# Performance work log

Hardware: AMD Instinct MI355X
Metric: run time of the kernel (lower is better)

The kernel has to match this reference:

```python
import jax, jax.numpy as jnp
import numpy as np

NUM_COMPONENTS = 8
STRIDE, PADDING, OUTPUT_PADDING, K = 2, 1, 0, 4


def get_comp_mat(n):
    # Cayley-Dickson construction: entry [i, j] = +/- component index of the
    # weight multiplying input component j to produce output component i.
    A = np.array([[0]])
    while A.shape[0] < n:
        m = A.shape[0]
        A = np.vstack([np.hstack([A, -(A + m)]), np.hstack([A + m, A])])
    return A


def setup_inputs() -> dict:
    key = jax.random.key(0)
    k1, k2, k3 = jax.random.split(key, 3)
    B, Cin, Cout, H = 8, 512, 256, 64
    c_in, c_out = Cin // NUM_COMPONENTS, Cout // NUM_COMPONENTS
    x = jax.random.normal(k1, (B, Cin, H, H), jnp.float32)
    # per-component ConvTranspose2d weights, torch layout [C_in, C_out, kH, kW]
    W = jax.random.normal(k2, (NUM_COMPONENTS, c_in, c_out, K, K), jnp.float32) * 0.05
    b = jax.random.normal(k3, (NUM_COMPONENTS, c_out), jnp.float32) * 0.05
    return {"x": x, "W": W, "b": b}


def reference(x, W, b):
    n = NUM_COMPONENTS
    comp = get_comp_mat(n)                 # static [n, n] signed component table
    signs = jnp.asarray(np.where(comp < 0, -1.0, 1.0), x.dtype)
    idx = np.abs(comp)                     # which sub-conv weight to use
    c_in, c_out, kh, kw = W.shape[1:]
    # Fuse the n^2 transpose convs into ONE block transpose conv:
    # Kbig[j*c_in:(j+1)*c_in, i*c_out:(i+1)*c_out] = sign[i,j] * W[idx[i,j]]
    Wsel = W[idx] * signs[:, :, None, None, None, None]          # [ni, nj, c_in, c_out, kh, kw]
    Wbig = jnp.transpose(Wsel, (1, 2, 0, 3, 4, 5)).reshape(n * c_in, n * c_out, kh, kw)
    bbig = jnp.einsum('ij,ijc->ic', signs, b[idx]).reshape(n * c_out)
    # torch ConvTranspose2d == conv with input dilated by stride and flipped kernel
    rhs = jnp.flip(Wbig, (2, 3)).transpose(1, 0, 2, 3)           # OIHW
    pad = K - 1 - PADDING
    out = jax.lax.conv_general_dilated(
        x, rhs, window_strides=(1, 1),
        padding=((pad, pad + OUTPUT_PADDING), (pad, pad + OUTPUT_PADDING)),
        lhs_dilation=(STRIDE, STRIDE),
        dimension_numbers=('NCHW', 'OIHW', 'NCHW'))
    return out + bbig[None, :, None, None]
```

## Files before the change

kernel.cpp:

```cpp
#include <hip/hip_runtime.h>
#include <hip/hip_bf16.h>

typedef unsigned short ushort_t;
typedef __attribute__((ext_vector_type(8))) short short8;
typedef __attribute__((ext_vector_type(4))) float f32x4;

#define NCOMP    8
#define CIN      512
#define COUT     256
#define H        64
#define HP       66
#define OHW      128
#define NB       8

__device__ const int d_idx8[8][8] = {
    {0,1,2,1,4,3,2,3},
    {1,0,3,2,5,4,1,2},
    {2,1,0,1,6,5,4,3},
    {3,2,1,0,7,6,5,4},
    {4,3,2,3,0,1,2,1},
    {5,4,1,2,1,0,3,2},
    {6,5,4,3,2,1,0,1},
    {7,6,5,4,3,2,1,0}};

__device__ const int kh_tab[2][2] = {{1,3},{0,2}};
__device__ const int dh_tab[2][2] = {{0,-1},{1,0}};

__global__ void prep_x(const float* __restrict__ x, ushort_t* __restrict__ xpadT) {
    __shared__ ushort_t tile[32][33];
    const int ih  = blockIdx.x;
    const int iw0 = (blockIdx.y & 1) * 32;
    const int ic0 = (blockIdx.y >> 1) * 32;
    const int b   = blockIdx.z;
    const int t   = threadIdx.x;

    for (int e = t; e < 1024; e += 256) {
        int icl = e >> 5, iwl = e & 31;
        float v = x[(((size_t)b * CIN + ic0 + icl) * H + ih) * H + iw0 + iwl];
        __hip_bfloat16 h = __float2bfloat16(v);
        tile[icl][iwl] = *(ushort_t*)&h;
    }
    __syncthreads();
    const int iwl = t >> 3, g = t & 7;
    ushort4 v;
    v.x = tile[g * 4 + 0][iwl];
    v.y = tile[g * 4 + 1][iwl];
    v.z = tile[g * 4 + 2][iwl];
    v.w = tile[g * 4 + 3][iwl];
    ushort_t* dst = xpadT + (((size_t)b * HP + ih + 1) * HP + iw0 + iwl + 1) * CIN + ic0 + g * 4;
    *(ushort4*)dst = v;
}

__global__ void prep_w(const float* __restrict__ W, const float* __restrict__ bias,
                       ushort_t* __restrict__ Abf, float* __restrict__ bbig) {
    const int t = blockIdx.x * blockDim.x + threadIdx.x;
    if (t < 4 * 64 * 256 * 32) {
        int kin = t & 31;
        int oc  = (t >> 5) & 255;
        int ks  = (t >> 13) & 63;
        int cls = t >> 19;
        int k  = ks * 32 + kin;
        int a  = k >> 10, c = (k >> 9) & 1, ic = k & 511;
        int ph = cls >> 1, pw = cls & 1;
        int kh = kh_tab[ph][a], kw = kh_tab[pw][c];
        int i = oc >> 5, co = oc & 31;
        int j = ic >> 6, ci = ic & 63;
        float s = (i >= j) ? 1.0f : -1.0f;
        float v = s * W[(((size_t)(d_idx8[i][j] * 64 + ci) * 32 + co) * 4 + kh) * 4 + kw];
        __hip_bfloat16 h = __float2bfloat16(v);
        Abf[t] = *(ushort_t*)&h;
    }
    if (t < COUT) {
        int i = t >> 5, co = t & 31;
        float acc = 0.0f;
        for (int j = 0; j < NCOMP; ++j)
            acc += ((i >= j) ? 1.0f : -1.0f) * bias[d_idx8[i][j] * 32 + co];
        bbig[t] = acc;
    }
}

__device__ __forceinline__ void async16(void* lds_dst, const void* g_src) {
    __builtin_amdgcn_global_load_lds(
        (const __attribute__((address_space(1))) unsigned int*)g_src,
        (__attribute__((address_space(3))) unsigned int*)lds_dst,
        16, 0, 0);
}

__launch_bounds__(256)
__global__ void htconv_mfma(const ushort_t* __restrict__ xpadT,
                            const ushort_t* __restrict__ Abf,
                            const float* __restrict__ bbig,
                            float* __restrict__ out) {
    __shared__ __align__(16) ushort_t smem[8192];
    char* sb = (char*)smem;

    const int t     = threadIdx.x;
    const int ntile = blockIdx.x;
    const int mtile = blockIdx.y;
    const int cls   = blockIdx.z & 3;
    const int b     = blockIdx.z >> 2;
    const int ph = cls >> 1, pw = cls & 1;
    const int ohh0 = ntile * 2;

    const int srcc = (((t & 3) ^ ((t >> 3) & 3)) * 8);
    const int m_a  = t >> 2;
    const ushort_t* ap = Abf + (((size_t)cls * 64) * 256 + (size_t)mtile * 128 + m_a) * 32 + srcc;

    const int dh0 = dh_tab[ph][0], dh1 = dh_tab[ph][1];
    const int dw0 = dh_tab[pw][0], dw1 = dh_tab[pw][1];
    const int oww = t >> 2;
    const ushort_t* bp[2][2][2];
#pragma unroll
    for (int a = 0; a < 2; ++a) {
        int dh = (a == 0) ? dh0 : dh1;
#pragma unroll
        for (int c = 0; c < 2; ++c) {
            int dw = (c == 0) ? dw0 : dw1;
#pragma unroll
            for (int row = 0; row < 2; ++row) {
                size_t idx = (((size_t)b * HP + ohh0 + row + dh + 1) * HP + oww + dw + 1) * CIN + srcc;
                bp[a][c][row] = xpadT + idx;
            }
        }
    }

    const int lane = t & 63, wave = t >> 6;
    const int wm = wave >> 1, wn = wave & 1;
    const int col = lane & 15, quad = lane >> 4;
    const int soff = (quad ^ ((col >> 1) & 3)) * 16;
    const int aoff = (wm * 64 + col) * 64 + soff;
    const int boff = 8192 + (wn * 64 + col) * 64 + soff;

    f32x4 acc[4][4];
#pragma unroll
    for (int i = 0; i < 4; ++i)
#pragma unroll
        for (int j = 0; j < 4; ++j)
            acc[i][j] = (f32x4){0.f, 0.f, 0.f, 0.f};

#pragma unroll
    for (int a = 0; a < 2; ++a) {
#pragma unroll
        for (int c = 0; c < 2; ++c) {
            const ushort_t* b0 = bp[a][c][0];
            const ushort_t* b1 = bp[a][c][1];
            for (int kk = 0; kk < 16; ++kk) {
                async16(sb + t * 16,         ap);
                async16(sb + 4096 + t * 16,  ap + 2048);
                async16(sb + 8192 + t * 16,  b0);
                async16(sb + 12288 + t * 16, b1);
                ap += 8192; b0 += 32; b1 += 32;
                __syncthreads();

                short8 af[4], bf[4];
#pragma unroll
                for (int s = 0; s < 4; ++s) {
                    af[s] = *(const short8*)(sb + aoff + s * 1024);
                    bf[s] = *(const short8*)(sb + boff + s * 1024);
                }
#pragma unroll
                for (int sm = 0; sm < 4; ++sm)
#pragma unroll
                    for (int sn = 0; sn < 4; ++sn)
                        acc[sm][sn] = __builtin_amdgcn_mfma_f32_16x16x32_bf16(
                            af[sm], bf[sn], acc[sm][sn], 0, 0, 0);
                __syncthreads();
            }
        }
    }

    const int oh = 2 * (ohh0 + wn) + ph;
#pragma unroll
    for (int sm = 0; sm < 4; ++sm) {
#pragma unroll
        for (int r = 0; r < 4; ++r) {
            const int occ = mtile * 128 + wm * 64 + sm * 16 + quad * 4 + r;
            const float bv = bbig[occ];
            float* obase = out + (((size_t)b * COUT + occ) * OHW + oh) * OHW + pw;
#pragma unroll
            for (int sn = 0; sn < 4; ++sn) {
                const int owi = sn * 16 + col;
                obase[2 * owi] = acc[sm][sn][r] + bv;
            }
        }
    }
}

extern "C" void kernel_launch(void* const* d_in, const int* in_sizes, int n_in,
                              void* d_out, int out_size, void* d_ws, size_t ws_size,
                              hipStream_t stream) {
    const float* x    = (const float*)d_in[0];
    const float* W    = (const float*)d_in[1];
    const float* bias = (const float*)d_in[2];
    float* out = (float*)d_out;

    ushort_t* xpadT = (ushort_t*)d_ws;
    ushort_t* Abf   = xpadT + (size_t)NB * HP * HP * CIN;
    float*    bbig  = (float*)(Abf + (size_t)4 * 64 * 256 * 32);

    hipMemsetAsync(xpadT, 0, (size_t)NB * HP * HP * CIN * sizeof(ushort_t), stream);
    prep_x<<<dim3(H, 32, NB), 256, 0, stream>>>(x, xpadT);
    prep_w<<<dim3((4 * 64 * 256 * 32) / 256), 256, 0, stream>>>(W, bias, Abf, bbig);
    htconv_mfma<<<dim3(32, 2, 32), 256, 0, stream>>>(xpadT, Abf, bbig, out);
}
```

Baseline: 372.5 us.

## Double-buffer LDS in conv GEMM main loop and zero only the padding halo

The MFMA main loop now uses two LDS buffers, so the async global-to-LDS loads for the next K-step are issued before the MFMAs on the current step. Each step ends with a single waitcnt and barrier instead of two syncthreads, and B-tile addresses are computed from two base pointers plus an offset. Separately, the full memset of the padded input buffer is replaced by a small kernel that writes zeros only to the halo rows and columns, cutting about 35MB of memset traffic. This doubles LDS use per block, which may lower occupancy.

```diff
diff --git a/kernel.cpp b/kernel.cpp
--- a/kernel.cpp
+++ b/kernel.cpp
@@ -25,6 +25,31 @@
 
 __device__ const int kh_tab[2][2] = {{1,3},{0,2}};
 __device__ const int dh_tab[2][2] = {{0,-1},{1,0}};
+
+__global__ void zero_halo(ushort_t* __restrict__ xpadT) {
+    const int t = blockIdx.x * 256 + threadIdx.x;
+    const int nA = 8 * 2 * 66 * 64;
+    short8 z = {0, 0, 0, 0, 0, 0, 0, 0};
+    if (t < nA) {
+        int v  = t & 63;
+        int r  = t >> 6;
+        int iw = r % 66;
+        int q  = r / 66;
+        int ih = (q & 1) * 65;
+        int b  = q >> 1;
+        *(short8*)(xpadT + (((size_t)b * HP + ih) * HP + iw) * CIN + v * 8) = z;
+    } else {
+        int u  = t - nA;
+        int v  = u & 63;
+        int r  = u >> 6;
+        int e  = r & 1;
+        int q  = r >> 1;
+        int ih = (q & 63) + 1;
+        int b  = q >> 6;
+        int iw = e * 65;
+        *(short8*)(xpadT + (((size_t)b * HP + ih) * HP + iw) * CIN + v * 8) = z;
+    }
+}
 
 __global__ void prep_x(const float* __restrict__ x, ushort_t* __restrict__ xpadT) {
     __shared__ ushort_t tile[32][33];
@@ -86,12 +111,43 @@
         16, 0, 0);
 }
 
+#define KSTEP(STEP, CB_CUR, CB_NXT)                                            \
+  {                                                                            \
+    const int ns = (STEP) + 1;                                                 \
+    if (ns < 64) {                                                             \
+      const int na  = ns >> 5;                                                 \
+      const int ncb = (ns >> 4) & 1;                                           \
+      const int go  = ((na ? dh1 : dh0) * HP + (ncb ? dw1 : dw0)) * CIN        \
+                      + (ns & 15) * 32;                                        \
+      const ushort_t* nap = Abf_t + (size_t)ns * 8192;                         \
+      async16(sb + (CB_NXT) + t * 16,         nap);                            \
+      async16(sb + (CB_NXT) + 4096 + t * 16,  nap + 2048);                     \
+      async16(sb + (CB_NXT) + 8192 + t * 16,  base_r0 + go);                   \
+      async16(sb + (CB_NXT) + 12288 + t * 16, base_r1 + go);                   \
+    }                                                                          \
+    short8 af[4], bf[4];                                                       \
+    _Pragma("unroll")                                                          \
+    for (int s = 0; s < 4; ++s) {                                              \
+      af[s] = *(const short8*)(sb + (CB_CUR) + aoff + s * 1024);               \
+      bf[s] = *(const short8*)(sb + (CB_CUR) + boff + s * 1024);               \
+    }                                                                          \
+    _Pragma("unroll")                                                          \
+    for (int sm = 0; sm < 4; ++sm)                                             \
+      _Pragma("unroll")                                                        \
+      for (int sn = 0; sn < 4; ++sn)                                           \
+        acc[sm][sn] = __builtin_amdgcn_mfma_f32_16x16x32_bf16(                 \
+            af[sm], bf[sn], acc[sm][sn], 0, 0, 0);                             \
+    asm volatile("s_waitcnt vmcnt(0) lgkmcnt(0)" ::: "memory");                \
+    __builtin_amdgcn_s_barrier();                                              \
+    __builtin_amdgcn_sched_barrier(0);                                         \
+  }
+
 __launch_bounds__(256)
 __global__ void htconv_mfma(const ushort_t* __restrict__ xpadT,
                             const ushort_t* __restrict__ Abf,
                             const float* __restrict__ bbig,
                             float* __restrict__ out) {
-    __shared__ __align__(16) ushort_t smem[8192];
+    __shared__ __align__(16) ushort_t smem[16384];
     char* sb = (char*)smem;
 
     const int t     = threadIdx.x;
@@ -104,25 +160,16 @@
 
     const int srcc = (((t & 3) ^ ((t >> 3) & 3)) * 8);
     const int m_a  = t >> 2;
-    const ushort_t* ap = Abf + (((size_t)cls * 64) * 256 + (size_t)mtile * 128 + m_a) * 32 + srcc;
+    const ushort_t* Abf_t =
+        Abf + (((size_t)cls * 64) * 256 + (size_t)mtile * 128 + m_a) * 32 + srcc;
 
     const int dh0 = dh_tab[ph][0], dh1 = dh_tab[ph][1];
     const int dw0 = dh_tab[pw][0], dw1 = dh_tab[pw][1];
     const int oww = t >> 2;
-    const ushort_t* bp[2][2][2];
-#pragma unroll
-    for (int a = 0; a < 2; ++a) {
-        int dh = (a == 0) ? dh0 : dh1;
-#pragma unroll
-        for (int c = 0; c < 2; ++c) {
-            int dw = (c == 0) ? dw0 : dw1;
-#pragma unroll
-            for (int row = 0; row < 2; ++row) {
-                size_t idx = (((size_t)b * HP + ohh0 + row + dh + 1) * HP + oww + dw + 1) * CIN + srcc;
-                bp[a][c][row] = xpadT + idx;
-            }
-        }
-    }
+    const ushort_t* base_r0 =
+        xpadT + (((size_t)b * HP + ohh0 + 0 + 1) * HP + oww + 1) * CIN + srcc;
+    const ushort_t* base_r1 =
+        xpadT + (((size_t)b * HP + ohh0 + 1 + 1) * HP + oww + 1) * CIN + srcc;
 
     const int lane = t & 63, wave = t >> 6;
     const int wm = wave >> 1, wn = wave & 1;
@@ -138,35 +185,21 @@
         for (int j = 0; j < 4; ++j)
             acc[i][j] = (f32x4){0.f, 0.f, 0.f, 0.f};
 
-#pragma unroll
-    for (int a = 0; a < 2; ++a) {
-#pragma unroll
-        for (int c = 0; c < 2; ++c) {
-            const ushort_t* b0 = bp[a][c][0];
-            const ushort_t* b1 = bp[a][c][1];
-            for (int kk = 0; kk < 16; ++kk) {
-                async16(sb + t * 16,         ap);
-                async16(sb + 4096 + t * 16,  ap + 2048);
-                async16(sb + 8192 + t * 16,  b0);
-                async16(sb + 12288 + t * 16, b1);
-                ap += 8192; b0 += 32; b1 += 32;
-                __syncthreads();
-
-                short8 af[4], bf[4];
-#pragma unroll
-                for (int s = 0; s < 4; ++s) {
-                    af[s] = *(const short8*)(sb + aoff + s * 1024);
-                    bf[s] = *(const short8*)(sb + boff + s * 1024);
-                }
-#pragma unroll
-                for (int sm = 0; sm < 4; ++sm)
-#pragma unroll
-                    for (int sn = 0; sn < 4; ++sn)
-                        acc[sm][sn] = __builtin_amdgcn_mfma_f32_16x16x32_bf16(
-                            af[sm], bf[sn], acc[sm][sn], 0, 0, 0);
-                __syncthreads();
-            }
-        }
+    {
+        const int go0 = (dh0 * HP + dw0) * CIN;
+        async16(sb + t * 16,         Abf_t);
+        async16(sb + 4096 + t * 16,  Abf_t + 2048);
+        async16(sb + 8192 + t * 16,  base_r0 + go0);
+        async16(sb + 12288 + t * 16, base_r1 + go0);
+    }
+    asm volatile("s_waitcnt vmcnt(0)" ::: "memory");
+    __builtin_amdgcn_s_barrier();
+    __builtin_amdgcn_sched_barrier(0);
+
+#pragma unroll 1
+    for (int sp = 0; sp < 32; ++sp) {
+        KSTEP(2 * sp,     0,     16384);
+        KSTEP(2 * sp + 1, 16384, 0);
     }
 
     const int oh = 2 * (ohh0 + wn) + ph;
@@ -198,7 +231,7 @@
     ushort_t* Abf   = xpadT + (size_t)NB * HP * HP * CIN;
     float*    bbig  = (float*)(Abf + (size_t)4 * 64 * 256 * 32);
 
-    hipMemsetAsync(xpadT, 0, (size_t)NB * HP * HP * CIN * sizeof(ushort_t), stream);
+    zero_halo<<<dim3(520), 256, 0, stream>>>(xpadT);
     prep_x<<<dim3(H, 32, NB), 256, 0, stream>>>(x, xpadT);
     prep_w<<<dim3((4 * 64 * 256 * 32) / 256), 256, 0, stream>>>(W, bias, Abf, bbig);
     htconv_mfma<<<dim3(32, 2, 32), 256, 0, stream>>>(xpadT, Abf, bbig, out);
```

Result: faster. 357.2 us (-4.1%).
